# Performance work log

Measured on AMD Instinct MI355X. Metric: run time of the kernel, lower is better.

## Reference

```python
import jax, jax.numpy as jnp
import numpy as np

B, C, H, W = 16, 256, 128, 128
K = 7
EPS = 1e-5


def conv2d(x, w, pad):
    # x [B,Ci,H,W], w [Co,Ci,kh,kw] -> NCHW conv, stride 1
    return jax.lax.conv_general_dilated(
        x, w, window_strides=(1, 1), padding=[(pad, pad), (pad, pad)],
        dimension_numbers=("NCHW", "OIHW", "NCHW"))


def grid_sample_bilinear(feat, grid):
    """torch.F.grid_sample(mode='bilinear', padding_mode='zeros', align_corners=False).
    feat [B,C,H,W], grid [B,H,W,2] with (x,y) in [-1,1]. Returns [B,C,H,W]."""
    b, c, h, w = feat.shape
    ix = ((grid[..., 0] + 1.0) * w - 1.0) * 0.5  # unnormalize, align_corners=False
    iy = ((grid[..., 1] + 1.0) * h - 1.0) * 0.5
    x0 = jnp.floor(ix)
    y0 = jnp.floor(iy)
    x1 = x0 + 1.0
    y1 = y0 + 1.0
    wx1 = ix - x0
    wx0 = 1.0 - wx1
    wy1 = iy - y0
    wy0 = 1.0 - wy1
    feat_flat = feat.reshape(b, c, h * w)

    def gather(xi, yi):
        xi_i = xi.astype(jnp.int32)
        yi_i = yi.astype(jnp.int32)
        valid = ((xi_i >= 0) & (xi_i < w) & (yi_i >= 0) & (yi_i < h)).astype(feat.dtype)
        xc = jnp.clip(xi_i, 0, w - 1)
        yc = jnp.clip(yi_i, 0, h - 1)
        idx = (yc * w + xc).reshape(b, 1, h * w)
        vals = jnp.take_along_axis(feat_flat, jnp.broadcast_to(idx, (b, c, h * w)), axis=2)
        return vals.reshape(b, c, h, w) * valid[:, None]

    out = (gather(x0, y0) * (wx0 * wy0)[:, None]
           + gather(x1, y0) * (wx1 * wy0)[:, None]
           + gather(x0, y1) * (wx0 * wy1)[:, None]
           + gather(x1, y1) * (wx1 * wy1)[:, None])
    return out


def setup_inputs() -> dict:
    key = jax.random.key(0)
    ks = jax.random.split(key, 5)
    return {
        "x": jax.random.normal(ks[0], (B, C, H, W), jnp.float32),
        "w1": jax.random.normal(ks[1], (16, 2, 3, 3), jnp.float32) * 0.1,
        "bn_gamma": jnp.ones((16,), jnp.float32),
        "bn_beta": jnp.zeros((16,), jnp.float32),
        "bn_mean": jnp.zeros((16,), jnp.float32),
        "bn_var": jnp.ones((16,), jnp.float32),
        "w2": jax.random.normal(ks[2], (2 * K * K, 16, 3, 3), jnp.float32) * 0.05,
        "b2": jax.random.normal(ks[3], (2 * K * K,), jnp.float32) * 0.05,
        "attn_w": jax.random.normal(ks[4], (1, 2, K, K), jnp.float32) * 0.1,
    }


def reference(x, w1, bn_gamma, bn_beta, bn_mean, bn_var, w2, b2, attn_w):
    # CBAM-style spatial descriptor
    avg = jnp.mean(x, axis=1, keepdims=True)
    mx = jnp.max(x, axis=1, keepdims=True)
    sf = jnp.concatenate([avg, mx], axis=1)  # [B,2,H,W]

    # offset branch: conv3x3 -> BN(eval) -> ReLU -> conv3x3(+bias)
    h1 = conv2d(sf, w1, 1)
    scale = (bn_gamma * jax.lax.rsqrt(bn_var + EPS))[None, :, None, None]
    h1 = jax.nn.relu((h1 - bn_mean[None, :, None, None]) * scale + bn_beta[None, :, None, None])
    off = conv2d(h1, w2, 1) + b2[None, :, None, None]  # [B,2*K*K,H,W]

    b_, _, h_, w_ = off.shape
    off = off.reshape(b_, 2, K * K, h_, w_).mean(axis=2)  # [B,2,H,W]
    off = jnp.tanh(off) * 0.5
    off = jnp.transpose(off, (0, 2, 3, 1))  # [B,H,W,2]

    gy, gx = jnp.meshgrid(jnp.linspace(-1.0, 1.0, h_, dtype=sf.dtype),
                          jnp.linspace(-1.0, 1.0, w_, dtype=sf.dtype), indexing="ij")
    base = jnp.stack([gx, gy], axis=-1)[None]  # [1,H,W,2]
    grid = jnp.clip(base + off, -1.0, 1.0)

    sampled = grid_sample_bilinear(sf, grid)  # [B,2,H,W]
    attn = conv2d(sampled, attn_w, K // 2)  # [B,1,H,W]
    return jax.nn.sigmoid(attn)
```

## Files before the change

kernel.cpp:

```cpp
#include <hip/hip_runtime.h>
#include <math.h>

#define B_  16
#define C_  256
#define H_  128
#define W_  128
#define HW  16384
#define KK  7

__global__ __launch_bounds__(256) void k_reduce_c(const float* __restrict__ x,
                                                  float* __restrict__ sf) {
    int t = blockIdx.x * 256 + threadIdx.x;
    int b = t >> 12;
    int p = t & 4095;
    const float4* xp = (const float4*)x + (size_t)b * (C_ * 4096) + p;

    float4 s0 = make_float4(0.f, 0.f, 0.f, 0.f), s1 = s0, s2 = s0, s3 = s0;
    const float NI = -3.402823466e+38f;
    float4 m0 = make_float4(NI, NI, NI, NI), m1 = m0, m2 = m0, m3 = m0;

    for (int c = 0; c < C_; c += 4) {
        float4 v0 = xp[(size_t)(c + 0) * 4096];
        float4 v1 = xp[(size_t)(c + 1) * 4096];
        float4 v2 = xp[(size_t)(c + 2) * 4096];
        float4 v3 = xp[(size_t)(c + 3) * 4096];
        s0.x += v0.x; s0.y += v0.y; s0.z += v0.z; s0.w += v0.w;
        s1.x += v1.x; s1.y += v1.y; s1.z += v1.z; s1.w += v1.w;
        s2.x += v2.x; s2.y += v2.y; s2.z += v2.z; s2.w += v2.w;
        s3.x += v3.x; s3.y += v3.y; s3.z += v3.z; s3.w += v3.w;
        m0.x = fmaxf(m0.x, v0.x); m0.y = fmaxf(m0.y, v0.y); m0.z = fmaxf(m0.z, v0.z); m0.w = fmaxf(m0.w, v0.w);
        m1.x = fmaxf(m1.x, v1.x); m1.y = fmaxf(m1.y, v1.y); m1.z = fmaxf(m1.z, v1.z); m1.w = fmaxf(m1.w, v1.w);
        m2.x = fmaxf(m2.x, v2.x); m2.y = fmaxf(m2.y, v2.y); m2.z = fmaxf(m2.z, v2.z); m2.w = fmaxf(m2.w, v2.w);
        m3.x = fmaxf(m3.x, v3.x); m3.y = fmaxf(m3.y, v3.y); m3.z = fmaxf(m3.z, v3.z); m3.w = fmaxf(m3.w, v3.w);
    }
    float4 s, m;
    s.x = (s0.x + s1.x) + (s2.x + s3.x);
    s.y = (s0.y + s1.y) + (s2.y + s3.y);
    s.z = (s0.z + s1.z) + (s2.z + s3.z);
    s.w = (s0.w + s1.w) + (s2.w + s3.w);
    m.x = fmaxf(fmaxf(m0.x, m1.x), fmaxf(m2.x, m3.x));
    m.y = fmaxf(fmaxf(m0.y, m1.y), fmaxf(m2.y, m3.y));
    m.z = fmaxf(fmaxf(m0.z, m1.z), fmaxf(m2.z, m3.z));
    m.w = fmaxf(fmaxf(m0.w, m1.w), fmaxf(m2.w, m3.w));
    const float inv = 1.0f / 256.0f;
    s.x *= inv; s.y *= inv; s.z *= inv; s.w *= inv;

    float4* o = (float4*)sf;
    o[(size_t)b * 8192 + p]        = s;
    o[(size_t)b * 8192 + 4096 + p] = m;
}

__global__ void k_wreduce(const float* __restrict__ w2, const float* __restrict__ b2,
                          float* __restrict__ w2r, float* __restrict__ b2r) {
    int tid = threadIdx.x;
    if (tid < 288) {
        int c = tid / 144;
        int r = tid % 144;
        float s = 0.f;
        for (int j = 0; j < 49; ++j) s += w2[(size_t)(c * 49 + j) * 144 + r];
        w2r[tid] = s * (1.0f / 49.0f);
    } else if (tid < 290) {
        int c = tid - 288;
        float s = 0.f;
        for (int j = 0; j < 49; ++j) s += b2[c * 49 + j];
        b2r[c] = s * (1.0f / 49.0f);
    }
}

__global__ __launch_bounds__(256) void k_off_sample(const float* __restrict__ sf,
                                                    const float* __restrict__ w1,
                                                    const float* __restrict__ gamma,
                                                    const float* __restrict__ beta,
                                                    const float* __restrict__ mean,
                                                    const float* __restrict__ var,
                                                    const float* __restrict__ w2r,
                                                    const float* __restrict__ b2r,
                                                    float* __restrict__ sampled) {
    __shared__ float sft[2][20][20];
    __shared__ float h1t[16][18][18];
    __shared__ float wl1[288], wl2[288];
    __shared__ float sc[16], bi[16], bl[2];

    int tid = threadIdx.x;
    for (int i = tid; i < 288; i += 256) { wl1[i] = w1[i]; wl2[i] = w2r[i]; }
    if (tid < 16) {
        float s = gamma[tid] * rsqrtf(var[tid] + 1e-5f);
        sc[tid] = s;
        bi[tid] = beta[tid] - mean[tid] * s;
    }
    if (tid < 2) bl[tid] = b2r[tid];

    int blk = blockIdx.x;
    int b   = blk >> 6;
    int t8  = blk & 63;
    int ty0 = (t8 >> 3) << 4;
    int tx0 = (t8 & 7) << 4;
    const float* sfb = sf + ((size_t)b << 15);

    for (int i = tid; i < 400; i += 256) {
        int ly = i / 20, lx = i % 20;
        int gy = ty0 + ly - 2, gx = tx0 + lx - 2;
        bool ok = (gy >= 0) & (gy < H_) & (gx >= 0) & (gx < W_);
        int gidx = gy * W_ + gx;
        sft[0][ly][lx] = ok ? sfb[gidx]      : 0.f;
        sft[1][ly][lx] = ok ? sfb[HW + gidx] : 0.f;
    }
    __syncthreads();

    for (int i = tid; i < 324; i += 256) {
        int ly = i / 18, lx = i % 18;
        int gy = ty0 + ly - 1, gx = tx0 + lx - 1;
        bool inside = (gy >= 0) & (gy < H_) & (gx >= 0) & (gx < W_);
        float in[2][9];
#pragma unroll
        for (int c = 0; c < 2; ++c)
#pragma unroll
            for (int kh = 0; kh < 3; ++kh)
#pragma unroll
                for (int kw = 0; kw < 3; ++kw)
                    in[c][kh * 3 + kw] = sft[c][ly + kh][lx + kw];
#pragma unroll
        for (int oc = 0; oc < 16; ++oc) {
            float acc = 0.f;
#pragma unroll
            for (int c = 0; c < 2; ++c)
#pragma unroll
                for (int k = 0; k < 9; ++k)
                    acc += in[c][k] * wl1[oc * 18 + c * 9 + k];
            h1t[oc][ly][lx] = inside ? fmaxf(acc * sc[oc] + bi[oc], 0.f) : 0.f;
        }
    }
    __syncthreads();

    int ly = tid >> 4, lx = tid & 15;
    float off0 = bl[0], off1 = bl[1];
#pragma unroll 4
    for (int ci = 0; ci < 16; ++ci) {
#pragma unroll
        for (int kh = 0; kh < 3; ++kh)
#pragma unroll
            for (int kw = 0; kw < 3; ++kw) {
                float v = h1t[ci][ly + kh][lx + kw];
                off0 += v * wl2[ci * 9 + kh * 3 + kw];
                off1 += v * wl2[144 + ci * 9 + kh * 3 + kw];
            }
    }
    off0 = tanhf(off0) * 0.5f;
    off1 = tanhf(off1) * 0.5f;

    int h = ty0 + ly, w = tx0 + lx;
    float gx = fmaf((float)w, 2.0f / 127.0f, -1.0f) + off0;
    float gy = fmaf((float)h, 2.0f / 127.0f, -1.0f) + off1;
    gx = fminf(fmaxf(gx, -1.0f), 1.0f);
    gy = fminf(fmaxf(gy, -1.0f), 1.0f);

    float ix = (gx + 1.0f) * 64.0f - 0.5f;
    float iy = (gy + 1.0f) * 64.0f - 0.5f;
    float x0f = floorf(ix), y0f = floorf(iy);
    int x0 = (int)x0f, y0 = (int)y0f;
    int x1 = x0 + 1,  y1 = y0 + 1;
    float wx1 = ix - x0f, wx0 = 1.0f - wx1;
    float wy1 = iy - y0f, wy0 = 1.0f - wy1;

    float o0 = 0.f, o1 = 0.f;
    if (x0 >= 0 && x0 < W_ && y0 >= 0 && y0 < H_) {
        int idx = y0 * W_ + x0; float wt = wx0 * wy0;
        o0 += sfb[idx] * wt; o1 += sfb[HW + idx] * wt;
    }
    if (x1 >= 0 && x1 < W_ && y0 >= 0 && y0 < H_) {
        int idx = y0 * W_ + x1; float wt = wx1 * wy0;
        o0 += sfb[idx] * wt; o1 += sfb[HW + idx] * wt;
    }
    if (x0 >= 0 && x0 < W_ && y1 >= 0 && y1 < H_) {
        int idx = y1 * W_ + x0; float wt = wx0 * wy1;
        o0 += sfb[idx] * wt; o1 += sfb[HW + idx] * wt;
    }
    if (x1 >= 0 && x1 < W_ && y1 >= 0 && y1 < H_) {
        int idx = y1 * W_ + x1; float wt = wx1 * wy1;
        o0 += sfb[idx] * wt; o1 += sfb[HW + idx] * wt;
    }
    int hw = h * W_ + w;
    sampled[((size_t)b << 15) + hw]      = o0;
    sampled[((size_t)b << 15) + HW + hw] = o1;
}

__global__ __launch_bounds__(256) void k_attn(const float* __restrict__ sampled,
                                              const float* __restrict__ aw,
                                              float* __restrict__ out) {
    __shared__ float tile[2][22][22];
    __shared__ float wl[98];
    int tid = threadIdx.x;
    if (tid < 98) wl[tid] = aw[tid];

    int blk = blockIdx.x;
    int b   = blk >> 6;
    int t8  = blk & 63;
    int ty0 = (t8 >> 3) << 4;
    int tx0 = (t8 & 7) << 4;
    const float* sb = sampled + ((size_t)b << 15);

    for (int i = tid; i < 484; i += 256) {
        int ly = i / 22, lx = i % 22;
        int gy = ty0 + ly - 3, gx = tx0 + lx - 3;
        bool ok = (gy >= 0) & (gy < H_) & (gx >= 0) & (gx < W_);
        int gidx = gy * W_ + gx;
        tile[0][ly][lx] = ok ? sb[gidx]      : 0.f;
        tile[1][ly][lx] = ok ? sb[HW + gidx] : 0.f;
    }
    __syncthreads();

    int ly = tid >> 4, lx = tid & 15;
    float acc = 0.f;
#pragma unroll
    for (int c = 0; c < 2; ++c)
#pragma unroll
        for (int ky = 0; ky < KK; ++ky)
#pragma unroll
            for (int kx = 0; kx < KK; ++kx)
                acc += tile[c][ly + ky][lx + kx] * wl[c * 49 + ky * 7 + kx];

    int h = ty0 + ly, w = tx0 + lx;
    out[((size_t)b << 14) + h * W_ + w] = 1.0f / (1.0f + expf(-acc));
}

extern "C" void kernel_launch(void* const* d_in, const int* in_sizes, int n_in,
                              void* d_out, int out_size, void* d_ws, size_t ws_size,
                              hipStream_t stream) {
    const float* x     = (const float*)d_in[0];
    const float* w1    = (const float*)d_in[1];
    const float* bn_g  = (const float*)d_in[2];
    const float* bn_b  = (const float*)d_in[3];
    const float* bn_m  = (const float*)d_in[4];
    const float* bn_v  = (const float*)d_in[5];
    const float* w2    = (const float*)d_in[6];
    const float* b2    = (const float*)d_in[7];
    const float* aw    = (const float*)d_in[8];
    float* out = (float*)d_out;

    float* ws = (float*)d_ws;
    float* sf      = ws;
    float* sampled = sf + (size_t)B_ * 2 * HW;
    float* w2r     = sampled + (size_t)B_ * 2 * HW;
    float* b2r     = w2r + 288;

    k_reduce_c<<<B_ * HW / 4 / 256, 256, 0, stream>>>(x, sf);
    k_wreduce<<<1, 320, 0, stream>>>(w2, b2, w2r, b2r);
    k_off_sample<<<B_ * 64, 256, 0, stream>>>(sf, w1, bn_g, bn_b, bn_m, bn_v,
                                              w2r, b2r, sampled);
    k_attn<<<B_ * 64, 256, 0, stream>>>(sampled, aw, out);
}
```

Before: 406.0 us.

## Split channel reduction across two half-blocks and fold weight reduction into same launch

The channel mean/max reduction now uses 512-thread blocks in which two halves each reduce 128 channels for the same pixels and combine their results through shared memory. This doubles the number of in-flight loads per pixel, and each thread issues eight loads per loop iteration instead of four. The separate single-block weight-reduction kernel moves into an extra block of the same launch, removing one kernel launch. The cost is a block-level barrier plus shared memory, and the weight block now runs alongside the reduction blocks rather than as its own launch.

After: 412.2 us. Within noise of the previous version (+1.5%).

```diff
diff --git a/kernel.cpp b/kernel.cpp
--- a/kernel.cpp
+++ b/kernel.cpp
@@ -8,31 +8,77 @@
 #define HW  16384
 #define KK  7
 
-__global__ __launch_bounds__(256) void k_reduce_c(const float* __restrict__ x,
-                                                  float* __restrict__ sf) {
-    int t = blockIdx.x * 256 + threadIdx.x;
-    int b = t >> 12;
-    int p = t & 4095;
-    const float4* xp = (const float4*)x + (size_t)b * (C_ * 4096) + p;
+__global__ __launch_bounds__(512) void k_stage1(const float* __restrict__ x,
+                                                const float* __restrict__ w2,
+                                                const float* __restrict__ b2,
+                                                float* __restrict__ sf,
+                                                float* __restrict__ w2r,
+                                                float* __restrict__ b2r) {
+    if (blockIdx.x == 256) {
+        int tid = threadIdx.x;
+        if (tid < 288) {
+            int c = tid / 144;
+            int r = tid % 144;
+            float s = 0.f;
+            for (int j = 0; j < 49; ++j) s += w2[(size_t)(c * 49 + j) * 144 + r];
+            w2r[tid] = s * (1.0f / 49.0f);
+        } else if (tid < 290) {
+            int c = tid - 288;
+            float s = 0.f;
+            for (int j = 0; j < 49; ++j) s += b2[c * 49 + j];
+            b2r[c] = s * (1.0f / 49.0f);
+        }
+        return;
+    }
+
+    __shared__ float4 ls[256];
+    __shared__ float4 lm[256];
+
+    int tid  = threadIdx.x;
+    int lane = tid & 255;
+    int half = tid >> 8;
+    int pos  = blockIdx.x * 256 + lane;
+    int b    = pos >> 12;
+    int p    = pos & 4095;
+
+    const float4* xp = (const float4*)x
+                     + (size_t)b * (C_ * 4096)
+                     + (size_t)(half * 128) * 4096
+                     + p;
 
     float4 s0 = make_float4(0.f, 0.f, 0.f, 0.f), s1 = s0, s2 = s0, s3 = s0;
     const float NI = -3.402823466e+38f;
     float4 m0 = make_float4(NI, NI, NI, NI), m1 = m0, m2 = m0, m3 = m0;
 
-    for (int c = 0; c < C_; c += 4) {
+    for (int c = 0; c < 128; c += 8) {
         float4 v0 = xp[(size_t)(c + 0) * 4096];
         float4 v1 = xp[(size_t)(c + 1) * 4096];
         float4 v2 = xp[(size_t)(c + 2) * 4096];
         float4 v3 = xp[(size_t)(c + 3) * 4096];
+        float4 v4 = xp[(size_t)(c + 4) * 4096];
+        float4 v5 = xp[(size_t)(c + 5) * 4096];
+        float4 v6 = xp[(size_t)(c + 6) * 4096];
+        float4 v7 = xp[(size_t)(c + 7) * 4096];
+
         s0.x += v0.x; s0.y += v0.y; s0.z += v0.z; s0.w += v0.w;
         s1.x += v1.x; s1.y += v1.y; s1.z += v1.z; s1.w += v1.w;
         s2.x += v2.x; s2.y += v2.y; s2.z += v2.z; s2.w += v2.w;
         s3.x += v3.x; s3.y += v3.y; s3.z += v3.z; s3.w += v3.w;
+        s0.x += v4.x; s0.y += v4.y; s0.z += v4.z; s0.w += v4.w;
+        s1.x += v5.x; s1.y += v5.y; s1.z += v5.z; s1.w += v5.w;
+        s2.x += v6.x; s2.y += v6.y; s2.z += v6.z; s2.w += v6.w;
+        s3.x += v7.x; s3.y += v7.y; s3.z += v7.z; s3.w += v7.w;
+
         m0.x = fmaxf(m0.x, v0.x); m0.y = fmaxf(m0.y, v0.y); m0.z = fmaxf(m0.z, v0.z); m0.w = fmaxf(m0.w, v0.w);
         m1.x = fmaxf(m1.x, v1.x); m1.y = fmaxf(m1.y, v1.y); m1.z = fmaxf(m1.z, v1.z); m1.w = fmaxf(m1.w, v1.w);
         m2.x = fmaxf(m2.x, v2.x); m2.y = fmaxf(m2.y, v2.y); m2.z = fmaxf(m2.z, v2.z); m2.w = fmaxf(m2.w, v2.w);
         m3.x = fmaxf(m3.x, v3.x); m3.y = fmaxf(m3.y, v3.y); m3.z = fmaxf(m3.z, v3.z); m3.w = fmaxf(m3.w, v3.w);
-    }
+        m0.x = fmaxf(m0.x, v4.x); m0.y = fmaxf(m0.y, v4.y); m0.z = fmaxf(m0.z, v4.z); m0.w = fmaxf(m0.w, v4.w);
+        m1.x = fmaxf(m1.x, v5.x); m1.y = fmaxf(m1.y, v5.y); m1.z = fmaxf(m1.z, v5.z); m1.w = fmaxf(m1.w, v5.w);
+        m2.x = fmaxf(m2.x, v6.x); m2.y = fmaxf(m2.y, v6.y); m2.z = fmaxf(m2.z, v6.z); m2.w = fmaxf(m2.w, v6.w);
+        m3.x = fmaxf(m3.x, v7.x); m3.y = fmaxf(m3.y, v7.y); m3.z = fmaxf(m3.z, v7.z); m3.w = fmaxf(m3.w, v7.w);
+    }
+
     float4 s, m;
     s.x = (s0.x + s1.x) + (s2.x + s3.x);
     s.y = (s0.y + s1.y) + (s2.y + s3.y);
@@ -42,28 +88,21 @@
     m.y = fmaxf(fmaxf(m0.y, m1.y), fmaxf(m2.y, m3.y));
     m.z = fmaxf(fmaxf(m0.z, m1.z), fmaxf(m2.z, m3.z));
     m.w = fmaxf(fmaxf(m0.w, m1.w), fmaxf(m2.w, m3.w));
-    const float inv = 1.0f / 256.0f;
-    s.x *= inv; s.y *= inv; s.z *= inv; s.w *= inv;
-
-    float4* o = (float4*)sf;
-    o[(size_t)b * 8192 + p]        = s;
-    o[(size_t)b * 8192 + 4096 + p] = m;
-}
-
-__global__ void k_wreduce(const float* __restrict__ w2, const float* __restrict__ b2,
-                          float* __restrict__ w2r, float* __restrict__ b2r) {
-    int tid = threadIdx.x;
-    if (tid < 288) {
-        int c = tid / 144;
-        int r = tid % 144;
-        float s = 0.f;
-        for (int j = 0; j < 49; ++j) s += w2[(size_t)(c * 49 + j) * 144 + r];
-        w2r[tid] = s * (1.0f / 49.0f);
-    } else if (tid < 290) {
-        int c = tid - 288;
-        float s = 0.f;
-        for (int j = 0; j < 49; ++j) s += b2[c * 49 + j];
-        b2r[c] = s * (1.0f / 49.0f);
+
+    if (half == 1) { ls[lane] = s; lm[lane] = m; }
+    __syncthreads();
+    if (half == 0) {
+        float4 s2_ = ls[lane];
+        float4 m2_ = lm[lane];
+        const float inv = 1.0f / 256.0f;
+        s.x = (s.x + s2_.x) * inv; s.y = (s.y + s2_.y) * inv;
+        s.z = (s.z + s2_.z) * inv; s.w = (s.w + s2_.w) * inv;
+        m.x = fmaxf(m.x, m2_.x); m.y = fmaxf(m.y, m2_.y);
+        m.z = fmaxf(m.z, m2_.z); m.w = fmaxf(m.w, m2_.w);
+
+        float4* o = (float4*)sf;
+        o[(size_t)b * 8192 + p]        = s;
+        o[(size_t)b * 8192 + 4096 + p] = m;
     }
 }
 
@@ -243,8 +282,7 @@
     float* w2r     = sampled + (size_t)B_ * 2 * HW;
     float* b2r     = w2r + 288;
 
-    k_reduce_c<<<B_ * HW / 4 / 256, 256, 0, stream>>>(x, sf);
-    k_wreduce<<<1, 320, 0, stream>>>(w2, b2, w2r, b2r);
+    k_stage1<<<257, 512, 0, stream>>>(x, w2, b2, sf, w2r, b2r);
     k_off_sample<<<B_ * 64, 256, 0, stream>>>(sf, w1, bn_g, bn_b, bn_m, bn_v,
                                               w2r, b2r, sampled);
     k_attn<<<B_ * 64, 256, 0, stream>>>(sampled, aw, out);
```
